# Optimization experiments

Measured on AMD Instinct MI355X. Metric: run time of the kernel, lower is better.

## Reference

```python
import jax, jax.numpy as jnp
import numpy as np

WINDOW_SIZE = 11
SIGMA = 1.5
C1 = 0.01 ** 2
C2 = 0.03 ** 2


def _gaussian_window(channel, dtype):
    # 1D gaussian, normalized, then outer product -> 2D window, expanded per channel
    xs = np.arange(WINDOW_SIZE) - WINDOW_SIZE // 2
    g = np.exp(-(xs.astype(np.float64) ** 2) / (2.0 * SIGMA ** 2))
    g = (g / g.sum()).astype(np.float32)
    w2d = np.outer(g, g)  # [ws, ws]
    w = np.broadcast_to(w2d[None, None], (channel, 1, WINDOW_SIZE, WINDOW_SIZE))
    return jnp.asarray(w, dtype=dtype)


def _depthwise_conv(img, window, channel):
    pad = WINDOW_SIZE // 2
    return jax.lax.conv_general_dilated(
        img, window,
        window_strides=(1, 1),
        padding=[(pad, pad), (pad, pad)],
        dimension_numbers=('NCHW', 'OIHW', 'NCHW'),
        feature_group_count=channel)


def setup_inputs() -> dict:
    key = jax.random.key(0)
    k1, k2 = jax.random.split(key)
    shape = (16, 3, 512, 512)
    x = jax.random.uniform(k1, shape, dtype=jnp.float32)
    y = jax.random.uniform(k2, shape, dtype=jnp.float32)
    return {"x": x, "y": y}


def reference(x, y):
    channel = x.shape[-3]
    window = _gaussian_window(channel, x.dtype)

    mu1 = _depthwise_conv(x, window, channel)
    mu2 = _depthwise_conv(y, window, channel)
    mu1_sq = mu1 * mu1
    mu2_sq = mu2 * mu2
    mu1_mu2 = mu1 * mu2
    sigma1_sq = _depthwise_conv(x * x, window, channel) - mu1_sq
    sigma2_sq = _depthwise_conv(y * y, window, channel) - mu2_sq
    sigma12 = _depthwise_conv(x * y, window, channel) - mu1_mu2

    ssim_map = ((2.0 * mu1_mu2 + C1) * (2.0 * sigma12 + C2)) / (
        (mu1_sq + mu2_sq + C1) * (sigma1_sq + sigma2_sq + C2))
    # DSSIM = 1 - mean(ssim)
    return 1.0 - jnp.mean(ssim_map)
```

## Files before the change

### kernel.cpp

```cpp
#include <hip/hip_runtime.h>


typedef _Float16 half8 __attribute__((ext_vector_type(8)));
typedef __fp16 pk16 __attribute__((ext_vector_type(2)));
typedef float f32x4 __attribute__((ext_vector_type(4)));
typedef float f32x8 __attribute__((ext_vector_type(8)));

#define IMG_W   512
#define IMG_H   512
#define NPLANES 48
#define BR      16
#define GRX     (IMG_H / BR)
#define NBLK    (GRX * NPLANES)

__global__ __launch_bounds__(256, 3)
void dssim_main(const float* __restrict__ xin, const float* __restrict__ yin,
                float* __restrict__ partial) {
    __shared__ float wpart[4];

    const int t    = threadIdx.x;
    const int lane = t & 63;
    const int wid  = t >> 6;
    const int bn   = lane & 15;
    const int jg   = lane >> 4;
    const int r0   = blockIdx.x * BR;
    const bool edge = (blockIdx.x == 0) || (blockIdx.x == GRX - 1);
    const size_t pbase = (size_t)blockIdx.y * (IMG_W * IMG_H);
    const float* __restrict__ xp = xin + pbase;
    const float* __restrict__ yp = yin + pbase;

    float ginv;
    {
        float s = 0.f;
#pragma unroll
        for (int i = 0; i < 11; ++i) {
            float d = (float)(i - 5);
            s += expf(-(d * d) * (1.0f / 4.5f));
        }
        ginv = 1.0f / s;
    }

    half8 whF, wvF;
#pragma unroll
    for (int j = 0; j < 8; ++j) {
        const int k = 8 * jg + j;
        const int dh = k - bn - 3;
        const int sigma = (j < 4) ? (4 * jg + j) : (12 + 4 * jg + j);
        const int dv = sigma - bn;
        float wh = 0.f, wv = 0.f;
        if (dh >= 0 && dh < 11) {
            const float d = (float)(dh - 5);
            wh = ginv * expf(-(d * d) * (1.0f / 4.5f));
        }
        if (dv >= 0 && dv < 11) {
            const float d = (float)(dv - 5);
            wv = ginv * expf(-(d * d) * (1.0f / 4.5f));
        }
        whF[j] = (_Float16)wh;
        wvF[j] = (_Float16)wv;
    }

    const int gr0 = r0 - 5 + bn;
    const bool rowok0 = (gr0 >= 0) && (gr0 < IMG_H);
    const int gr1 = r0 + 11 + bn;
    const bool rowok1 = (bn < 10) && (gr1 < IMG_H);
    const size_t row0 = (size_t)(rowok0 ? gr0 : 0) * IMG_W;
    const size_t row1 = (size_t)(rowok1 ? gr1 : 0) * IMG_W;

    const int cb = (wid << 4) + (jg << 3) - 8;
    const float* bx0 = xp + row0 + cb;
    const float* by0 = yp + row0 + cb;
    const float* bx1 = xp + row1 + cb;
    const float* by1 = yp + row1 + cb;

    const f32x8 z8 = {0.f, 0.f, 0.f, 0.f, 0.f, 0.f, 0.f, 0.f};
    const f32x4 zf = {0.f, 0.f, 0.f, 0.f};
    const float C1 = 0.0001f, C2 = 0.0009f;
    float lsum = 0.f;

    f32x8 xs0, ys0, xs1, ys1;
    half8 bU, bW, bP, bQ;

#define LOADP(m)                                                            \
    {                                                                       \
        int fix = 0;                                                        \
        if ((m) == 0) fix = (wid == 0 && jg == 0) ? 8 : 0;                  \
        if ((m) == 7) fix = (wid == 3 && jg == 3) ? -8 : 0;                 \
        const int off = 64 * (m);                                           \
        xs0 = *(const f32x8*)(bx0 + off + fix);                             \
        ys0 = *(const f32x8*)(by0 + off + fix);                             \
        xs1 = *(const f32x8*)(bx1 + off + fix);                             \
        ys1 = *(const f32x8*)(by1 + off + fix);                             \
        if ((m) == 0) {                                                     \
            if (wid == 0 && jg == 0) { xs0 = z8; ys0 = z8; xs1 = z8; ys1 = z8; } \
        }                                                                   \
        if ((m) == 7) {                                                     \
            if (wid == 3 && jg == 3) { xs0 = z8; ys0 = z8; xs1 = z8; ys1 = z8; } \
        }                                                                   \
        if (edge) {                                                         \
            if (!rowok0) { xs0 = z8; ys0 = z8; }                            \
            if (!rowok1) { xs1 = z8; ys1 = z8; }                            \
        }                                                                   \
    }

#define HCOMP()                                                             \
    {                                                                       \
        half8 aU0, aW0, aU1, aW1;                                           \
        _Pragma("unroll")                                                   \
        for (int d = 0; d < 4; ++d) {                                       \
            const pk16 pu0 = __builtin_amdgcn_cvt_pkrtz(                    \
                xs0[2 * d] + ys0[2 * d], xs0[2 * d + 1] + ys0[2 * d + 1]);  \
            const pk16 pw0 = __builtin_amdgcn_cvt_pkrtz(                    \
                xs0[2 * d] - ys0[2 * d], xs0[2 * d + 1] - ys0[2 * d + 1]);  \
            const pk16 pu1 = __builtin_amdgcn_cvt_pkrtz(                    \
                xs1[2 * d] + ys1[2 * d], xs1[2 * d + 1] + ys1[2 * d + 1]);  \
            const pk16 pw1 = __builtin_amdgcn_cvt_pkrtz(                    \
                xs1[2 * d] - ys1[2 * d], xs1[2 * d + 1] - ys1[2 * d + 1]);  \
            aU0[2 * d] = (_Float16)pu0[0]; aU0[2 * d + 1] = (_Float16)pu0[1]; \
            aW0[2 * d] = (_Float16)pw0[0]; aW0[2 * d + 1] = (_Float16)pw0[1]; \
            aU1[2 * d] = (_Float16)pu1[0]; aU1[2 * d + 1] = (_Float16)pu1[1]; \
            aW1[2 * d] = (_Float16)pw1[0]; aW1[2 * d + 1] = (_Float16)pw1[1]; \
        }                                                                   \
        const half8 aP0 = aU0 * aU0;                                        \
        const half8 aQ0 = aW0 * aW0;                                        \
        const half8 aP1 = aU1 * aU1;                                        \
        const half8 aQ1 = aW1 * aW1;                                        \
        const f32x4 cU0 = __builtin_amdgcn_mfma_f32_16x16x32_f16(aU0, whF, zf, 0, 0, 0); \
        const f32x4 cW0 = __builtin_amdgcn_mfma_f32_16x16x32_f16(aW0, whF, zf, 0, 0, 0); \
        const f32x4 cP0 = __builtin_amdgcn_mfma_f32_16x16x32_f16(aP0, whF, zf, 0, 0, 0); \
        const f32x4 cQ0 = __builtin_amdgcn_mfma_f32_16x16x32_f16(aQ0, whF, zf, 0, 0, 0); \
        const f32x4 cU1 = __builtin_amdgcn_mfma_f32_16x16x32_f16(aU1, whF, zf, 0, 0, 0); \
        const f32x4 cW1 = __builtin_amdgcn_mfma_f32_16x16x32_f16(aW1, whF, zf, 0, 0, 0); \
        const f32x4 cP1 = __builtin_amdgcn_mfma_f32_16x16x32_f16(aP1, whF, zf, 0, 0, 0); \
        const f32x4 cQ1 = __builtin_amdgcn_mfma_f32_16x16x32_f16(aQ1, whF, zf, 0, 0, 0); \
        _Pragma("unroll")                                                   \
        for (int q = 0; q < 2; ++q) {                                       \
            const pk16 u0 = __builtin_amdgcn_cvt_pkrtz(cU0[2*q], cU0[2*q+1]); \
            const pk16 w0 = __builtin_amdgcn_cvt_pkrtz(cW0[2*q], cW0[2*q+1]); \
            const pk16 p0 = __builtin_amdgcn_cvt_pkrtz(cP0[2*q], cP0[2*q+1]); \
            const pk16 q0 = __builtin_amdgcn_cvt_pkrtz(cQ0[2*q], cQ0[2*q+1]); \
            const pk16 u1 = __builtin_amdgcn_cvt_pkrtz(cU1[2*q], cU1[2*q+1]); \
            const pk16 w1 = __builtin_amdgcn_cvt_pkrtz(cW1[2*q], cW1[2*q+1]); \
            const pk16 p1 = __builtin_amdgcn_cvt_pkrtz(cP1[2*q], cP1[2*q+1]); \
            const pk16 q1 = __builtin_amdgcn_cvt_pkrtz(cQ1[2*q], cQ1[2*q+1]); \
            bU[2*q]     = (_Float16)u0[0]; bU[2*q + 1]     = (_Float16)u0[1]; \
            bW[2*q]     = (_Float16)w0[0]; bW[2*q + 1]     = (_Float16)w0[1]; \
            bP[2*q]     = (_Float16)p0[0]; bP[2*q + 1]     = (_Float16)p0[1]; \
            bQ[2*q]     = (_Float16)q0[0]; bQ[2*q + 1]     = (_Float16)q0[1]; \
            bU[2*q + 4] = (_Float16)u1[0]; bU[2*q + 5]     = (_Float16)u1[1]; \
            bW[2*q + 4] = (_Float16)w1[0]; bW[2*q + 5]     = (_Float16)w1[1]; \
            bP[2*q + 4] = (_Float16)p1[0]; bP[2*q + 5]     = (_Float16)p1[1]; \
            bQ[2*q + 4] = (_Float16)q1[0]; bQ[2*q + 5]     = (_Float16)q1[1]; \
        }                                                                   \
    }

#define VBLUR()                                                             \
    {                                                                       \
        const f32x4 accU = __builtin_amdgcn_mfma_f32_16x16x32_f16(wvF, bU, zf, 0, 0, 0); \
        const f32x4 accW = __builtin_amdgcn_mfma_f32_16x16x32_f16(wvF, bW, zf, 0, 0, 0); \
        const f32x4 accP = __builtin_amdgcn_mfma_f32_16x16x32_f16(wvF, bP, zf, 0, 0, 0); \
        const f32x4 accQ = __builtin_amdgcn_mfma_f32_16x16x32_f16(wvF, bQ, zf, 0, 0, 0); \
        _Pragma("unroll")                                                   \
        for (int q = 0; q < 4; ++q) {                                       \
            const float U = accU[q], W = accW[q];                           \
            const float P = accP[q], Q = accQ[q];                           \
            const float U2 = U * U, W2 = W * W;                             \
            const float A = 0.5f * (U2 + W2);                               \
            const float B = 0.5f * (U2 - W2);                               \
            const float den2 = fmaf(0.5f, P + Q, -A) + C2;                  \
            const float num2 = fmaf(0.5f, P - Q, -B) + C2;                  \
            lsum += (B + C1) * num2 * __builtin_amdgcn_rcpf((A + C1) * den2); \
        }                                                                   \
    }

    LOADP(0);
    HCOMP();
#pragma unroll
    for (int i = 0; i < 8; ++i) {
        if (i < 7) LOADP(i + 1);
        VBLUR();
        if (i < 7) HCOMP();
    }

#pragma unroll
    for (int off = 32; off >= 1; off >>= 1)
        lsum += __shfl_down(lsum, off, 64);
    if (lane == 0) wpart[wid] = lsum;
    __syncthreads();
    if (t == 0) {
        partial[(size_t)blockIdx.y * GRX + blockIdx.x] =
            wpart[0] + wpart[1] + wpart[2] + wpart[3];
    }
}

__global__ __launch_bounds__(256)
void dssim_final(const float* __restrict__ partial, float* __restrict__ out) {
    __shared__ double wsum[4];
    double s = 0.0;
    for (int i = threadIdx.x; i < NBLK; i += 256) s += (double)partial[i];
#pragma unroll
    for (int off = 32; off >= 1; off >>= 1)
        s += __shfl_down(s, off, 64);
    if ((threadIdx.x & 63) == 0) wsum[threadIdx.x >> 6] = s;
    __syncthreads();
    if (threadIdx.x == 0) {
        const double tot = wsum[0] + wsum[1] + wsum[2] + wsum[3];
        out[0] = (float)(1.0 - tot / 12582912.0);
    }
}

extern "C" void kernel_launch(void* const* d_in, const int* in_sizes, int n_in,
                              void* d_out, int out_size, void* d_ws, size_t ws_size,
                              hipStream_t stream) {
    const float* x = (const float*)d_in[0];
    const float* y = (const float*)d_in[1];
    float* out = (float*)d_out;
    float* partial = (float*)d_ws;

    dim3 grid(GRX, NPLANES);
    dim3 block(256);
    dssim_main<<<grid, block, 0, stream>>>(x, y, partial);
    dssim_final<<<1, block, 0, stream>>>(partial, out);
}
```

Baseline: 53.49 us.

## Double-buffer loads two stages ahead and convert inputs to fp16 before combining

```diff
diff --git a/kernel.cpp b/kernel.cpp
--- a/kernel.cpp
+++ b/kernel.cpp
@@ -13,7 +13,7 @@
 #define GRX     (IMG_H / BR)
 #define NBLK    (GRX * NPLANES)
 
-__global__ __launch_bounds__(256, 3)
+__global__
 void dssim_main(const float* __restrict__ xin, const float* __restrict__ yin,
                 float* __restrict__ partial) {
     __shared__ float wpart[4];
@@ -78,49 +78,51 @@
     const float C1 = 0.0001f, C2 = 0.0009f;
     float lsum = 0.f;
 
-    f32x8 xs0, ys0, xs1, ys1;
-    half8 bU, bW, bP, bQ;
-
-#define LOADP(m)                                                            \
+    f32x8 xsA0, ysA0, xsA1, ysA1, xsB0, ysB0, xsB1, ysB1;
+    half8 bUA, bWA, bPA, bQA, bUB, bWB, bPB, bQB;
+
+#define LOADP(m, S)                                                         \
     {                                                                       \
         int fix = 0;                                                        \
         if ((m) == 0) fix = (wid == 0 && jg == 0) ? 8 : 0;                  \
         if ((m) == 7) fix = (wid == 3 && jg == 3) ? -8 : 0;                 \
         const int off = 64 * (m);                                           \
-        xs0 = *(const f32x8*)(bx0 + off + fix);                             \
-        ys0 = *(const f32x8*)(by0 + off + fix);                             \
-        xs1 = *(const f32x8*)(bx1 + off + fix);                             \
-        ys1 = *(const f32x8*)(by1 + off + fix);                             \
+        xs##S##0 = *(const f32x8*)(bx0 + off + fix);                        \
+        ys##S##0 = *(const f32x8*)(by0 + off + fix);                        \
+        xs##S##1 = *(const f32x8*)(bx1 + off + fix);                        \
+        ys##S##1 = *(const f32x8*)(by1 + off + fix);                        \
         if ((m) == 0) {                                                     \
-            if (wid == 0 && jg == 0) { xs0 = z8; ys0 = z8; xs1 = z8; ys1 = z8; } \
+            if (wid == 0 && jg == 0) { xs##S##0 = z8; ys##S##0 = z8;        \
+                                       xs##S##1 = z8; ys##S##1 = z8; }      \
         }                                                                   \
         if ((m) == 7) {                                                     \
-            if (wid == 3 && jg == 3) { xs0 = z8; ys0 = z8; xs1 = z8; ys1 = z8; } \
+            if (wid == 3 && jg == 3) { xs##S##0 = z8; ys##S##0 = z8;        \
+                                       xs##S##1 = z8; ys##S##1 = z8; }      \
         }                                                                   \
         if (edge) {                                                         \
-            if (!rowok0) { xs0 = z8; ys0 = z8; }                            \
-            if (!rowok1) { xs1 = z8; ys1 = z8; }                            \
-        }                                                                   \
-    }
-
-#define HCOMP()                                                             \
+            if (!rowok0) { xs##S##0 = z8; ys##S##0 = z8; }                  \
+            if (!rowok1) { xs##S##1 = z8; ys##S##1 = z8; }                  \
+        }                                                                   \
+    }
+
+#define HCOMPM(S, F)                                                        \
     {                                                                       \
-        half8 aU0, aW0, aU1, aW1;                                           \
+        half8 hx0, hy0, hx1, hy1;                                           \
         _Pragma("unroll")                                                   \
         for (int d = 0; d < 4; ++d) {                                       \
-            const pk16 pu0 = __builtin_amdgcn_cvt_pkrtz(                    \
-                xs0[2 * d] + ys0[2 * d], xs0[2 * d + 1] + ys0[2 * d + 1]);  \
-            const pk16 pw0 = __builtin_amdgcn_cvt_pkrtz(                    \
-                xs0[2 * d] - ys0[2 * d], xs0[2 * d + 1] - ys0[2 * d + 1]);  \
-            const pk16 pu1 = __builtin_amdgcn_cvt_pkrtz(                    \
-                xs1[2 * d] + ys1[2 * d], xs1[2 * d + 1] + ys1[2 * d + 1]);  \
-            const pk16 pw1 = __builtin_amdgcn_cvt_pkrtz(                    \
-                xs1[2 * d] - ys1[2 * d], xs1[2 * d + 1] - ys1[2 * d + 1]);  \
-            aU0[2 * d] = (_Float16)pu0[0]; aU0[2 * d + 1] = (_Float16)pu0[1]; \
-            aW0[2 * d] = (_Float16)pw0[0]; aW0[2 * d + 1] = (_Float16)pw0[1]; \
-            aU1[2 * d] = (_Float16)pu1[0]; aU1[2 * d + 1] = (_Float16)pu1[1]; \
-            aW1[2 * d] = (_Float16)pw1[0]; aW1[2 * d + 1] = (_Float16)pw1[1]; \
-        }                                                                   \
+            const pk16 a0 = __builtin_amdgcn_cvt_pkrtz(xs##S##0[2*d], xs##S##0[2*d+1]); \
+            const pk16 b0 = __builtin_amdgcn_cvt_pkrtz(ys##S##0[2*d], ys##S##0[2*d+1]); \
+            const pk16 a1 = __builtin_amdgcn_cvt_pkrtz(xs##S##1[2*d], xs##S##1[2*d+1]); \
+            const pk16 b1 = __builtin_amdgcn_cvt_pkrtz(ys##S##1[2*d], ys##S##1[2*d+1]); \
+            hx0[2*d] = (_Float16)a0[0]; hx0[2*d+1] = (_Float16)a0[1];       \
+            hy0[2*d] = (_Float16)b0[0]; hy0[2*d+1] = (_Float16)b0[1];       \
+            hx1[2*d] = (_Float16)a1[0]; hx1[2*d+1] = (_Float16)a1[1];       \
+            hy1[2*d] = (_Float16)b1[0]; hy1[2*d+1] = (_Float16)b1[1];       \
+        }                                                                   \
+        const half8 aU0 = hx0 + hy0;                                        \
+        const half8 aW0 = hx0 - hy0;                                        \
+        const half8 aU1 = hx1 + hy1;                                        \
+        const half8 aW1 = hx1 - hy1;                                        \
         const half8 aP0 = aU0 * aU0;                                        \
         const half8 aQ0 = aW0 * aW0;                                        \
         const half8 aP1 = aU1 * aU1;                                        \
@@ -143,23 +145,23 @@
             const pk16 w1 = __builtin_amdgcn_cvt_pkrtz(cW1[2*q], cW1[2*q+1]); \
             const pk16 p1 = __builtin_amdgcn_cvt_pkrtz(cP1[2*q], cP1[2*q+1]); \
             const pk16 q1 = __builtin_amdgcn_cvt_pkrtz(cQ1[2*q], cQ1[2*q+1]); \
-            bU[2*q]     = (_Float16)u0[0]; bU[2*q + 1]     = (_Float16)u0[1]; \
-            bW[2*q]     = (_Float16)w0[0]; bW[2*q + 1]     = (_Float16)w0[1]; \
-            bP[2*q]     = (_Float16)p0[0]; bP[2*q + 1]     = (_Float16)p0[1]; \
-            bQ[2*q]     = (_Float16)q0[0]; bQ[2*q + 1]     = (_Float16)q0[1]; \
-            bU[2*q + 4] = (_Float16)u1[0]; bU[2*q + 5]     = (_Float16)u1[1]; \
-            bW[2*q + 4] = (_Float16)w1[0]; bW[2*q + 5]     = (_Float16)w1[1]; \
-            bP[2*q + 4] = (_Float16)p1[0]; bP[2*q + 5]     = (_Float16)p1[1]; \
-            bQ[2*q + 4] = (_Float16)q1[0]; bQ[2*q + 5]     = (_Float16)q1[1]; \
-        }                                                                   \
-    }
-
-#define VBLUR()                                                             \
+            bU##F[2*q]   = (_Float16)u0[0]; bU##F[2*q+1] = (_Float16)u0[1]; \
+            bW##F[2*q]   = (_Float16)w0[0]; bW##F[2*q+1] = (_Float16)w0[1]; \
+            bP##F[2*q]   = (_Float16)p0[0]; bP##F[2*q+1] = (_Float16)p0[1]; \
+            bQ##F[2*q]   = (_Float16)q0[0]; bQ##F[2*q+1] = (_Float16)q0[1]; \
+            bU##F[2*q+4] = (_Float16)u1[0]; bU##F[2*q+5] = (_Float16)u1[1]; \
+            bW##F[2*q+4] = (_Float16)w1[0]; bW##F[2*q+5] = (_Float16)w1[1]; \
+            bP##F[2*q+4] = (_Float16)p1[0]; bP##F[2*q+5] = (_Float16)p1[1]; \
+            bQ##F[2*q+4] = (_Float16)q1[0]; bQ##F[2*q+5] = (_Float16)q1[1]; \
+        }                                                                   \
+    }
+
+#define VBLURM(F)                                                           \
     {                                                                       \
-        const f32x4 accU = __builtin_amdgcn_mfma_f32_16x16x32_f16(wvF, bU, zf, 0, 0, 0); \
-        const f32x4 accW = __builtin_amdgcn_mfma_f32_16x16x32_f16(wvF, bW, zf, 0, 0, 0); \
-        const f32x4 accP = __builtin_amdgcn_mfma_f32_16x16x32_f16(wvF, bP, zf, 0, 0, 0); \
-        const f32x4 accQ = __builtin_amdgcn_mfma_f32_16x16x32_f16(wvF, bQ, zf, 0, 0, 0); \
+        const f32x4 accU = __builtin_amdgcn_mfma_f32_16x16x32_f16(wvF, bU##F, zf, 0, 0, 0); \
+        const f32x4 accW = __builtin_amdgcn_mfma_f32_16x16x32_f16(wvF, bW##F, zf, 0, 0, 0); \
+        const f32x4 accP = __builtin_amdgcn_mfma_f32_16x16x32_f16(wvF, bP##F, zf, 0, 0, 0); \
+        const f32x4 accQ = __builtin_amdgcn_mfma_f32_16x16x32_f16(wvF, bQ##F, zf, 0, 0, 0); \
         _Pragma("unroll")                                                   \
         for (int q = 0; q < 4; ++q) {                                       \
             const float U = accU[q], W = accW[q];                           \
@@ -173,14 +175,16 @@
         }                                                                   \
     }
 
-    LOADP(0);
-    HCOMP();
-#pragma unroll
-    for (int i = 0; i < 8; ++i) {
-        if (i < 7) LOADP(i + 1);
-        VBLUR();
-        if (i < 7) HCOMP();
-    }
+    LOADP(0, A); LOADP(1, B);
+    HCOMPM(A, A);
+     LOADP(2, A); HCOMPM(B, B); VBLURM(A);
+     LOADP(3, B); HCOMPM(A, A); VBLURM(B);
+     LOADP(4, A); HCOMPM(B, B); VBLURM(A);
+     LOADP(5, B); HCOMPM(A, A); VBLURM(B);
+     LOADP(6, A); HCOMPM(B, B); VBLURM(A);
+     LOADP(7, B); HCOMPM(A, A); VBLURM(B);
+                  HCOMPM(B, B); VBLURM(A);
+                                VBLURM(B);
 
 #pragma unroll
     for (int off = 32; off >= 1; off >>= 1)
```

Result: slower. 140.7 us (+163.0%).
